# Performance work log

Measured on AMD Instinct MI355X. Metric: run time of the kernel, lower is better.

## Reference

```python
import jax, jax.numpy as jnp
import numpy as np

N_SUB, N_GLOB, S, H = 32768, 65536, 1024, 256
E_SUB, E_GLOB = 262144, 1048576


def gcn_conv(x, edge_index, W, b):
    """PyG GCNConv: add self-loops, symmetric deg^-1/2 normalization, scatter-add to targets."""
    N = x.shape[0]
    loops = jnp.arange(N, dtype=edge_index.dtype)
    row = jnp.concatenate([edge_index[0], loops])  # source
    col = jnp.concatenate([edge_index[1], loops])  # target
    deg = jax.ops.segment_sum(jnp.ones(row.shape[0], x.dtype), col, num_segments=N)
    dis = jnp.where(deg > 0, jax.lax.rsqrt(deg), 0.0)
    norm = dis[row] * dis[col]  # [E+N]
    h = x @ W  # [N,H]
    msg = h[row] * norm[:, None]  # gather + scale
    out = jax.ops.segment_sum(msg, col, num_segments=N)  # scatter-add
    return out + b


def mean_pool(x, batch, num_segments):
    sums = jax.ops.segment_sum(x, batch, num_segments=num_segments)
    cnt = jax.ops.segment_sum(jnp.ones(x.shape[0], x.dtype), batch, num_segments=num_segments)
    return sums / jnp.maximum(cnt, 1.0)[:, None]


def setup_inputs() -> dict:
    key = jax.random.key(0)
    ks = jax.random.split(key, 10)
    x_sub = jax.random.normal(ks[0], (N_SUB, H), jnp.float32)
    edge_index_sub = jax.random.randint(ks[1], (2, E_SUB), 0, N_SUB, jnp.int32)
    batch_sub = jnp.repeat(jnp.arange(S, dtype=jnp.int32), N_SUB // S)  # 32 nodes/subgraph
    sub_index = jax.random.permutation(ks[2], N_GLOB)[:S].astype(jnp.int32)  # unique targets
    x_glob = jax.random.normal(ks[3], (N_GLOB, H), jnp.float32)
    edge_index_glob = jax.random.randint(ks[4], (2, E_GLOB), 0, N_GLOB, jnp.int32)
    batch_glob = jnp.zeros((N_GLOB,), jnp.int32)
    s = 1.0 / np.sqrt(H)
    W_sub = jax.random.uniform(ks[5], (H, H), jnp.float32, -s, s)
    b_sub = jnp.zeros((H,), jnp.float32)
    W_glob = jax.random.uniform(ks[6], (H, H), jnp.float32, -s, s)
    b_glob = jnp.zeros((H,), jnp.float32)
    fc_W = jax.random.uniform(ks[7], (H, H), jnp.float32, -s, s)
    fc_b = jax.random.uniform(ks[8], (H,), jnp.float32, -s, s)
    return dict(x_sub=x_sub, edge_index_sub=edge_index_sub, batch_sub=batch_sub,
                sub_index=sub_index, x_glob=x_glob, edge_index_glob=edge_index_glob,
                batch_glob=batch_glob, W_sub=W_sub, b_sub=b_sub, W_glob=W_glob,
                b_glob=b_glob, fc_W=fc_W, fc_b=fc_b)


def reference(x_sub, edge_index_sub, batch_sub, sub_index, x_glob, edge_index_glob,
              batch_glob, W_sub, b_sub, W_glob, b_glob, fc_W, fc_b):
    # subgraph conv + per-subgraph mean pool
    h_sub = jax.nn.relu(gcn_conv(x_sub, edge_index_sub, W_sub, b_sub))
    pooled = mean_pool(h_sub, batch_sub, S)  # [S,H]
    # inject pooled subgraph embeddings into global node features
    gx = x_glob.at[sub_index].add(pooled)
    # global conv + global mean pool (batch_glob is all zeros -> 1 graph)
    gh = jax.nn.relu(gcn_conv(gx, edge_index_glob, W_glob, b_glob))
    gemb = mean_pool(gh, batch_glob, 1)  # [1,H]
    return gemb @ fc_W.T + fc_b


if __name__ == "__main__":
    out = reference(**setup_inputs())
    print(out.shape)
```

## Files before the change

### kernel.cpp

```cpp
#include <hip/hip_runtime.h>
#include <math.h>

#define NSUB  32768
#define NGLOB 65536
#define SSUB  1024
#define HD    256
#define ESUB  262144
#define EGLOB 1048576

typedef short short8 __attribute__((ext_vector_type(8)));
typedef float f32x4 __attribute__((ext_vector_type(4)));

static __device__ __forceinline__ unsigned short f2b(float f) {
  unsigned int u = __float_as_uint(f);
  unsigned int r = (u + 0x7fffu + ((u >> 16) & 1u)) >> 16;
  return (unsigned short)r;
}
static __device__ __forceinline__ float b2f(unsigned short s) {
  return __uint_as_float(((unsigned int)s) << 16);
}


__global__ void k_init(int* __restrict__ ecnt_sub, int* __restrict__ ecnt_glob,
                       int* __restrict__ inv) {
  int i = blockIdx.x * blockDim.x + threadIdx.x;
  if (i < NSUB) ecnt_sub[i] = 0;
  ecnt_glob[i] = 0;
  inv[i] = -1;
}

__global__ void k_hist2(const int* __restrict__ col_s, const int* __restrict__ col_g,
                        int* __restrict__ cnt_s, int* __restrict__ cnt_g) {
  int i = blockIdx.x * blockDim.x + threadIdx.x;
  if (i < ESUB) atomicAdd(&cnt_s[col_s[i]], 1);
  else atomicAdd(&cnt_g[col_g[i - ESUB]], 1);
}

__global__ __launch_bounds__(256) void k_scanA(const int* __restrict__ cnt_s,
                                               const int* __restrict__ cnt_g,
                                               int* __restrict__ bsum) {
  const int b = blockIdx.x;
  const int t = threadIdx.x;
  const int* cnt = (b < 32) ? cnt_s : cnt_g;
  const int chunk = (b < 32) ? b : (b - 32);
  int4 v = *(const int4*)(cnt + chunk * 1024 + t * 4);
  int s = v.x + v.y + v.z + v.w;
  __shared__ int ls[4];
#pragma unroll
  for (int d = 32; d; d >>= 1) s += __shfl_down(s, d);
  if ((t & 63) == 0) ls[t >> 6] = s;
  __syncthreads();
  if (t == 0) bsum[b] = ls[0] + ls[1] + ls[2] + ls[3];
}

__global__ void k_scanB(const int* __restrict__ bsum, int* __restrict__ bbase) {
  __shared__ int s[96];
  int t = threadIdx.x;
  if (t < 96) s[t] = bsum[t];
  __syncthreads();
  if (t == 0) { int run = 0; for (int i = 0; i < 32; ++i) { int c = s[i]; s[i] = run; run += c; } }
  if (t == 1) { int run = 0; for (int i = 32; i < 96; ++i) { int c = s[i]; s[i] = run; run += c; } }
  __syncthreads();
  if (t < 96) bbase[t] = s[t];
}

__global__ __launch_bounds__(256) void k_scanC(const int* __restrict__ cnt_s,
                                               const int* __restrict__ cnt_g,
                                               const int* __restrict__ bbase,
                                               int* __restrict__ off_s, int* __restrict__ cur_s,
                                               float* __restrict__ dis_s,
                                               int* __restrict__ off_g, int* __restrict__ cur_g,
                                               float* __restrict__ dis_g) {
  const int b = blockIdx.x;
  const int t = threadIdx.x;
  const bool isS = (b < 32);
  const int chunk = isS ? b : (b - 32);
  const int* cnt = isS ? cnt_s : cnt_g;
  int* off = isS ? off_s : off_g;
  int* cur = isS ? cur_s : cur_g;
  float* dis = isS ? dis_s : dis_g;
  const int N = isS ? NSUB : NGLOB;
  const int base = bbase[b];
  const int i0 = chunk * 1024 + t * 4;
  int4 v = *(const int4*)(cnt + i0);
  int mysum = v.x + v.y + v.z + v.w;
  __shared__ int ss[256];
  ss[t] = mysum;
  __syncthreads();
  for (int d = 1; d < 256; d <<= 1) {
    int u = (t >= d) ? ss[t - d] : 0;
    __syncthreads();
    ss[t] += u;
    __syncthreads();
  }
  int pre = base + ((t == 0) ? 0 : ss[t - 1]);
  int4 o;
  o.x = pre;
  o.y = o.x + v.x;
  o.z = o.y + v.y;
  o.w = o.z + v.z;
  *(int4*)(off + i0) = o;
  *(int4*)(cur + i0) = o;
  float4 dd = make_float4(rsqrtf((float)(v.x + 1)), rsqrtf((float)(v.y + 1)),
                          rsqrtf((float)(v.z + 1)), rsqrtf((float)(v.w + 1)));
  *(float4*)(dis + i0) = dd;
  if (i0 + 4 == N) off[N] = o.w + v.w;
}

__global__ void k_scatter2(const int* __restrict__ row_s, const int* __restrict__ col_s,
                           const int* __restrict__ row_g, const int* __restrict__ col_g,
                           int* __restrict__ cur_s, int* __restrict__ cur_g,
                           int* __restrict__ src_s, int* __restrict__ src_g) {
  int i = blockIdx.x * blockDim.x + threadIdx.x;
  if (i < ESUB) {
    int c = col_s[i];
    int slot = atomicAdd(&cur_s[c], 1);
    src_s[slot] = row_s[i];
  } else {
    int j = i - ESUB;
    int c = col_g[j];
    int slot = atomicAdd(&cur_g[c], 1);
    src_g[slot] = row_g[j];
  }
}

__global__ void k_inv(const int* __restrict__ sub_index, int* __restrict__ inv) {
  int s = blockIdx.x * blockDim.x + threadIdx.x;
  if (s < SSUB) inv[sub_index[s]] = s;
}

__global__ void k_wt(const float* __restrict__ Ws, const float* __restrict__ Wg,
                     unsigned short* __restrict__ WtS, unsigned short* __restrict__ WtG) {
  int b = blockIdx.x;
  int k = threadIdx.x;
  if (b < 256) WtS[b * 256 + k] = f2b(Ws[k * 256 + b]);
  else {
    int n = b - 256;
    WtG[n * 256 + k] = f2b(Wg[k * 256 + n]);
  }
}

template <bool ADD_POOLED>
__global__ __launch_bounds__(512) void k_gemm(const float* __restrict__ X,
                                              const unsigned short* __restrict__ Wt,
                                              unsigned short* __restrict__ Hout,
                                              const float* __restrict__ dis,
                                              const int* __restrict__ inv,
                                              const float* __restrict__ pooled) {
  __shared__ __align__(16) char As[128 * 256 * 2];
  const int t = threadIdx.x;
  const int row0 = blockIdx.x * 128;

#pragma unroll
  for (int u = 0; u < 8; ++u) {
    int idx8 = u * 512 + t;
    int r = idx8 >> 5;
    int k8 = (idx8 & 31) * 8;
    const float* p = X + (size_t)(row0 + r) * HD + k8;
    float4 a = *(const float4*)p;
    float4 b = *(const float4*)(p + 4);
    if (ADD_POOLED) {
      int piv = inv[row0 + r];
      if (piv >= 0) {
        const float* pp = pooled + (size_t)piv * HD + k8;
        float4 pa = *(const float4*)pp;
        float4 pb = *(const float4*)(pp + 4);
        a.x += pa.x; a.y += pa.y; a.z += pa.z; a.w += pa.w;
        b.x += pb.x; b.y += pb.y; b.z += pb.z; b.w += pb.w;
      }
    }
    short8 h;
    h[0] = (short)f2b(a.x); h[1] = (short)f2b(a.y);
    h[2] = (short)f2b(a.z); h[3] = (short)f2b(a.w);
    h[4] = (short)f2b(b.x); h[5] = (short)f2b(b.y);
    h[6] = (short)f2b(b.z); h[7] = (short)f2b(b.w);
    int byte = r * 512 + ((k8 * 2) ^ ((r & 7) << 4));
    *(short8*)(As + byte) = h;
  }
  __syncthreads();

  const int wid = t >> 6;
  const int lane = t & 63;
  const int wr = wid >> 2;
  const int wc = wid & 3;
  const int l15 = lane & 15;
  const int l4 = lane >> 4;

  f32x4 acc[4][4];
#pragma unroll
  for (int m = 0; m < 4; ++m)
#pragma unroll
    for (int n = 0; n < 4; ++n) acc[m][n] = (f32x4){0.f, 0.f, 0.f, 0.f};

  const unsigned short* WtB = Wt + (size_t)(wc * 64 + l15) * HD + l4 * 8;

#pragma unroll
  for (int kk = 0; kk < 8; ++kk) {
    short8 bfrag[4];
#pragma unroll
    for (int n = 0; n < 4; ++n)
      bfrag[n] = *(const short8*)(WtB + (size_t)n * 16 * HD + kk * 32);
    short8 afrag[4];
#pragma unroll
    for (int m = 0; m < 4; ++m) {
      int r = wr * 64 + m * 16 + l15;
      int ke2 = (kk * 32 + l4 * 8) * 2;
      afrag[m] = *(const short8*)(As + r * 512 + (ke2 ^ ((r & 7) << 4)));
    }
#pragma unroll
    for (int m = 0; m < 4; ++m)
#pragma unroll
      for (int n = 0; n < 4; ++n)
        acc[m][n] = __builtin_amdgcn_mfma_f32_16x16x32_bf16(afrag[m], bfrag[n], acc[m][n], 0, 0, 0);
  }

#pragma unroll
  for (int m = 0; m < 4; ++m) {
    int rbase = row0 + wr * 64 + m * 16 + l4 * 4;
    float d0 = dis[rbase + 0], d1 = dis[rbase + 1];
    float d2 = dis[rbase + 2], d3 = dis[rbase + 3];
#pragma unroll
    for (int n = 0; n < 4; ++n) {
      int c = wc * 64 + n * 16 + l15;
      unsigned short* dst = Hout + (size_t)rbase * HD + c;
      dst[0 * HD] = f2b(acc[m][n][0] * d0);
      dst[1 * HD] = f2b(acc[m][n][1] * d1);
      dst[2 * HD] = f2b(acc[m][n][2] * d2);
      dst[3 * HD] = f2b(acc[m][n][3] * d3);
    }
  }
}

__global__ __launch_bounds__(256) void k_aggpool_sub(const unsigned short* __restrict__ hh,
                                                     const int* __restrict__ off,
                                                     const int* __restrict__ src,
                                                     const float* __restrict__ dis,
                                                     const float* __restrict__ bias,
                                                     float* __restrict__ psub) {
  const int ch = threadIdx.x;
  const int bid = blockIdx.x;
  const int base = (bid >> 2) * 32 + (bid & 3) * 8;
  const float bv = bias[ch];
  float psum = 0.f;
  for (int n = 0; n < 8; ++n) {
    const int c = base + n;
    float acc = b2f(hh[(size_t)c * HD + ch]);
    int e = off[c];
    const int e1 = off[c + 1];
    for (; e + 3 < e1; e += 4) {
      int r0 = src[e], r1 = src[e + 1], r2 = src[e + 2], r3 = src[e + 3];
      acc += b2f(hh[(size_t)r0 * HD + ch]) + b2f(hh[(size_t)r1 * HD + ch]) +
             b2f(hh[(size_t)r2 * HD + ch]) + b2f(hh[(size_t)r3 * HD + ch]);
    }
    for (; e < e1; ++e) acc += b2f(hh[(size_t)src[e] * HD + ch]);
    psum += fmaxf(dis[c] * acc + bv, 0.f);
  }
  psub[(size_t)bid * HD + ch] = psum;
}

__global__ void k_redpool(const float* __restrict__ psub, float* __restrict__ pooled) {
  const int ch = threadIdx.x;
  const int s = blockIdx.x;
  float v = psub[(size_t)(4 * s + 0) * HD + ch] + psub[(size_t)(4 * s + 1) * HD + ch] +
            psub[(size_t)(4 * s + 2) * HD + ch] + psub[(size_t)(4 * s + 3) * HD + ch];
  pooled[(size_t)s * HD + ch] = v * (1.f / 32.f);
}

__global__ __launch_bounds__(256) void k_aggsum_glob(const unsigned short* __restrict__ hh,
                                                     const int* __restrict__ off,
                                                     const int* __restrict__ src,
                                                     const float* __restrict__ dis,
                                                     const float* __restrict__ bias,
                                                     float* __restrict__ pg) {
  const int ch = threadIdx.x;
  const int bid = blockIdx.x;
  const float bv = bias[ch];
  float psum = 0.f;
  for (int n = 0; n < 16; ++n) {
    const int c = bid * 16 + n;
    float acc = b2f(hh[(size_t)c * HD + ch]);
    int e = off[c];
    const int e1 = off[c + 1];
    for (; e + 3 < e1; e += 4) {
      int r0 = src[e], r1 = src[e + 1], r2 = src[e + 2], r3 = src[e + 3];
      acc += b2f(hh[(size_t)r0 * HD + ch]) + b2f(hh[(size_t)r1 * HD + ch]) +
             b2f(hh[(size_t)r2 * HD + ch]) + b2f(hh[(size_t)r3 * HD + ch]);
    }
    for (; e < e1; ++e) acc += b2f(hh[(size_t)src[e] * HD + ch]);
    psum += fmaxf(dis[c] * acc + bv, 0.f);
  }
  pg[(size_t)bid * HD + ch] = psum;
}

__global__ void k_red1(const float* __restrict__ pg, float* __restrict__ p2) {
  const int ch = threadIdx.x;
  const int b = blockIdx.x;
  float v = 0.f;
  for (int i = 0; i < 16; ++i) v += pg[(size_t)(b * 16 + i) * HD + ch];
  p2[(size_t)b * HD + ch] = v;
}

__global__ void k_final(const float* __restrict__ p2, const float* __restrict__ fcW,
                        const float* __restrict__ fcb, float* __restrict__ out) {
  __shared__ float gemb[HD];
  const int ch = threadIdx.x;
  float s = 0.f;
  for (int i = 0; i < 256; ++i) s += p2[(size_t)i * HD + ch];
  gemb[ch] = s * (1.f / 65536.f);
  __syncthreads();
  float o = fcb[ch];
  const float* wr = fcW + (size_t)ch * HD;
  for (int j = 0; j < HD; ++j) o += wr[j] * gemb[j];
  out[ch] = o;
}

extern "C" void kernel_launch(void* const* d_in, const int* in_sizes, int n_in,
                              void* d_out, int out_size, void* d_ws, size_t ws_size,
                              hipStream_t stream) {
  (void)in_sizes; (void)n_in; (void)out_size; (void)ws_size;

  const float* x_sub    = (const float*)d_in[0];
  const int*   ei_sub   = (const int*)d_in[1];
  const int*   sub_index= (const int*)d_in[3];
  const float* x_glob   = (const float*)d_in[4];
  const int*   ei_glob  = (const int*)d_in[5];
  const float* W_sub    = (const float*)d_in[7];
  const float* b_sub    = (const float*)d_in[8];
  const float* W_glob   = (const float*)d_in[9];
  const float* b_glob   = (const float*)d_in[10];
  const float* fc_W     = (const float*)d_in[11];
  const float* fc_b     = (const float*)d_in[12];
  float* out = (float*)d_out;

  char* w = (char*)d_ws;
  auto nxt = [&](size_t b) -> void* {
    void* p = (void*)w;
    w += (b + 255) & ~(size_t)255;
    return p;
  };
  unsigned short* hs   = (unsigned short*)nxt(sizeof(short) * (size_t)NSUB * HD);
  unsigned short* hg   = (unsigned short*)nxt(sizeof(short) * (size_t)NGLOB * HD);
  unsigned short* wtS  = (unsigned short*)nxt(sizeof(short) * HD * HD);
  unsigned short* wtG  = (unsigned short*)nxt(sizeof(short) * HD * HD);
  float* psub   = (float*)nxt(sizeof(float) * 4096 * HD);
  float* pooled = (float*)nxt(sizeof(float) * SSUB * HD);
  float* pg     = (float*)nxt(sizeof(float) * 4096 * HD);
  float* p2     = (float*)nxt(sizeof(float) * 256 * HD);
  int* ecnt_s   = (int*)nxt(sizeof(int) * NSUB);
  float* dis_s  = (float*)nxt(sizeof(float) * NSUB);
  int* off_s    = (int*)nxt(sizeof(int) * (NSUB + 1));
  int* cur_s    = (int*)nxt(sizeof(int) * NSUB);
  int* src_s    = (int*)nxt(sizeof(int) * ESUB);
  int* ecnt_g   = (int*)nxt(sizeof(int) * NGLOB);
  float* dis_g  = (float*)nxt(sizeof(float) * NGLOB);
  int* off_g    = (int*)nxt(sizeof(int) * (NGLOB + 1));
  int* cur_g    = (int*)nxt(sizeof(int) * NGLOB);
  int* src_g    = (int*)nxt(sizeof(int) * EGLOB);
  int* inv      = (int*)nxt(sizeof(int) * NGLOB);
  int* bsum     = (int*)nxt(sizeof(int) * 96);
  int* bbase    = (int*)nxt(sizeof(int) * 96);

  const int* row_s = ei_sub;
  const int* col_s = ei_sub + ESUB;
  const int* row_g = ei_glob;
  const int* col_g = ei_glob + EGLOB;

  k_init<<<NGLOB / 256, 256, 0, stream>>>(ecnt_s, ecnt_g, inv);
  k_hist2<<<(ESUB + EGLOB) / 256, 256, 0, stream>>>(col_s, col_g, ecnt_s, ecnt_g);
  k_scanA<<<96, 256, 0, stream>>>(ecnt_s, ecnt_g, bsum);
  k_scanB<<<1, 128, 0, stream>>>(bsum, bbase);
  k_scanC<<<96, 256, 0, stream>>>(ecnt_s, ecnt_g, bbase,
                                  off_s, cur_s, dis_s, off_g, cur_g, dis_g);
  k_scatter2<<<(ESUB + EGLOB) / 256, 256, 0, stream>>>(row_s, col_s, row_g, col_g,
                                                       cur_s, cur_g, src_s, src_g);
  k_inv<<<SSUB / 256, 256, 0, stream>>>(sub_index, inv);
  k_wt<<<512, 256, 0, stream>>>(W_sub, W_glob, wtS, wtG);

  k_gemm<false><<<NSUB / 128, 512, 0, stream>>>(x_sub, wtS, hs, dis_s, nullptr, nullptr);
  k_aggpool_sub<<<4096, 256, 0, stream>>>(hs, off_s, src_s, dis_s, b_sub, psub);
  k_redpool<<<SSUB, 256, 0, stream>>>(psub, pooled);

  k_gemm<true><<<NGLOB / 128, 512, 0, stream>>>(x_glob, wtG, hg, dis_g, inv, pooled);
  k_aggsum_glob<<<4096, 256, 0, stream>>>(hg, off_g, src_g, dis_g, b_glob, pg);
  k_red1<<<256, 256, 0, stream>>>(pg, p2);
  k_final<<<1, 256, 0, stream>>>(p2, fc_W, fc_b, out);
}
```

Baseline: 501.8 us.

## Build CSR with two-level bucket scatter and local sort; widen gather unroll

Replaces the per-node global-atomic CSR scatter with a two-pass scheme. Edges are first scattered into 64-node buckets with a packed (local col, row) word, then each bucket is sorted into final slots using shared-memory atomics. This aims to reduce global atomic contention and random writes, at the cost of an extra pass and buffer. It also vectorises the histogram loads, unrolls the aggregation gathers by 8, and adds unroll pragmas to the reductions. The packing stores the row in 16 bits, but global rows go up to 65535, which still fits.

```diff
diff --git a/kernel.cpp b/kernel.cpp
--- a/kernel.cpp
+++ b/kernel.cpp
@@ -32,8 +32,16 @@
 __global__ void k_hist2(const int* __restrict__ col_s, const int* __restrict__ col_g,
                         int* __restrict__ cnt_s, int* __restrict__ cnt_g) {
   int i = blockIdx.x * blockDim.x + threadIdx.x;
-  if (i < ESUB) atomicAdd(&cnt_s[col_s[i]], 1);
-  else atomicAdd(&cnt_g[col_g[i - ESUB]], 1);
+  if (i < ESUB / 4) {
+    int4 c = *(const int4*)(col_s + i * 4);
+    atomicAdd(&cnt_s[c.x], 1); atomicAdd(&cnt_s[c.y], 1);
+    atomicAdd(&cnt_s[c.z], 1); atomicAdd(&cnt_s[c.w], 1);
+  } else {
+    int j = i - ESUB / 4;
+    int4 c = *(const int4*)(col_g + j * 4);
+    atomicAdd(&cnt_g[c.x], 1); atomicAdd(&cnt_g[c.y], 1);
+    atomicAdd(&cnt_g[c.z], 1); atomicAdd(&cnt_g[c.w], 1);
+  }
 }
 
 __global__ __launch_bounds__(256) void k_scanA(const int* __restrict__ cnt_s,
@@ -67,18 +75,18 @@
 __global__ __launch_bounds__(256) void k_scanC(const int* __restrict__ cnt_s,
                                                const int* __restrict__ cnt_g,
                                                const int* __restrict__ bbase,
-                                               int* __restrict__ off_s, int* __restrict__ cur_s,
-                                               float* __restrict__ dis_s,
-                                               int* __restrict__ off_g, int* __restrict__ cur_g,
-                                               float* __restrict__ dis_g) {
+                                               int* __restrict__ off_s, float* __restrict__ dis_s,
+                                               int* __restrict__ bcur_s,
+                                               int* __restrict__ off_g, float* __restrict__ dis_g,
+                                               int* __restrict__ bcur_g) {
   const int b = blockIdx.x;
   const int t = threadIdx.x;
   const bool isS = (b < 32);
   const int chunk = isS ? b : (b - 32);
   const int* cnt = isS ? cnt_s : cnt_g;
   int* off = isS ? off_s : off_g;
-  int* cur = isS ? cur_s : cur_g;
   float* dis = isS ? dis_s : dis_g;
+  int* bcur = isS ? bcur_s : bcur_g;
   const int N = isS ? NSUB : NGLOB;
   const int base = bbase[b];
   const int i0 = chunk * 1024 + t * 4;
@@ -100,27 +108,51 @@
   o.z = o.y + v.y;
   o.w = o.z + v.z;
   *(int4*)(off + i0) = o;
-  *(int4*)(cur + i0) = o;
+  if ((i0 & 63) == 0) bcur[i0 >> 6] = o.x;
   float4 dd = make_float4(rsqrtf((float)(v.x + 1)), rsqrtf((float)(v.y + 1)),
                           rsqrtf((float)(v.z + 1)), rsqrtf((float)(v.w + 1)));
   *(float4*)(dis + i0) = dd;
   if (i0 + 4 == N) off[N] = o.w + v.w;
 }
 
-__global__ void k_scatter2(const int* __restrict__ row_s, const int* __restrict__ col_s,
+__global__ void k_bscatter(const int* __restrict__ row_s, const int* __restrict__ col_s,
                            const int* __restrict__ row_g, const int* __restrict__ col_g,
-                           int* __restrict__ cur_s, int* __restrict__ cur_g,
-                           int* __restrict__ src_s, int* __restrict__ src_g) {
+                           int* __restrict__ bcur_s, int* __restrict__ bcur_g,
+                           unsigned int* __restrict__ ebuf_s, unsigned int* __restrict__ ebuf_g) {
   int i = blockIdx.x * blockDim.x + threadIdx.x;
   if (i < ESUB) {
-    int c = col_s[i];
-    int slot = atomicAdd(&cur_s[c], 1);
-    src_s[slot] = row_s[i];
+    int c = col_s[i], r = row_s[i];
+    int slot = atomicAdd(&bcur_s[c >> 6], 1);
+    ebuf_s[slot] = ((unsigned)(c & 63) << 16) | (unsigned)r;
   } else {
     int j = i - ESUB;
-    int c = col_g[j];
-    int slot = atomicAdd(&cur_g[c], 1);
-    src_g[slot] = row_g[j];
+    int c = col_g[j], r = row_g[j];
+    int slot = atomicAdd(&bcur_g[c >> 6], 1);
+    ebuf_g[slot] = ((unsigned)(c & 63) << 16) | (unsigned)r;
+  }
+}
+
+__global__ __launch_bounds__(256) void k_bsort(const unsigned int* __restrict__ ebuf_s,
+                                               const unsigned int* __restrict__ ebuf_g,
+                                               const int* __restrict__ off_s,
+                                               const int* __restrict__ off_g,
+                                               int* __restrict__ src_s, int* __restrict__ src_g) {
+  __shared__ int lcur[64];
+  const int b = blockIdx.x;
+  const bool isS = (b < 512);
+  const unsigned int* ebuf = isS ? ebuf_s : ebuf_g;
+  const int* off = isS ? off_s : off_g;
+  int* src = isS ? src_s : src_g;
+  const int node0 = (isS ? b : (b - 512)) * 64;
+  const int t = threadIdx.x;
+  if (t < 64) lcur[t] = off[node0 + t];
+  __syncthreads();
+  const int base = off[node0];
+  const int end = off[node0 + 64];
+  for (int i = base + t; i < end; i += 256) {
+    unsigned e = ebuf[i];
+    int slot = atomicAdd(&lcur[e >> 16], 1);
+    src[slot] = (int)(e & 0xFFFFu);
   }
 }
 
@@ -247,10 +279,13 @@
     float acc = b2f(hh[(size_t)c * HD + ch]);
     int e = off[c];
     const int e1 = off[c + 1];
-    for (; e + 3 < e1; e += 4) {
-      int r0 = src[e], r1 = src[e + 1], r2 = src[e + 2], r3 = src[e + 3];
-      acc += b2f(hh[(size_t)r0 * HD + ch]) + b2f(hh[(size_t)r1 * HD + ch]) +
-             b2f(hh[(size_t)r2 * HD + ch]) + b2f(hh[(size_t)r3 * HD + ch]);
+    const int n8 = e + ((e1 - e) & ~7);
+    for (; e < n8; e += 8) {
+      int r[8];
+#pragma unroll
+      for (int q = 0; q < 8; ++q) r[q] = src[e + q];
+#pragma unroll
+      for (int q = 0; q < 8; ++q) acc += b2f(hh[(size_t)r[q] * HD + ch]);
     }
     for (; e < e1; ++e) acc += b2f(hh[(size_t)src[e] * HD + ch]);
     psum += fmaxf(dis[c] * acc + bv, 0.f);
@@ -281,10 +316,13 @@
     float acc = b2f(hh[(size_t)c * HD + ch]);
     int e = off[c];
     const int e1 = off[c + 1];
-    for (; e + 3 < e1; e += 4) {
-      int r0 = src[e], r1 = src[e + 1], r2 = src[e + 2], r3 = src[e + 3];
-      acc += b2f(hh[(size_t)r0 * HD + ch]) + b2f(hh[(size_t)r1 * HD + ch]) +
-             b2f(hh[(size_t)r2 * HD + ch]) + b2f(hh[(size_t)r3 * HD + ch]);
+    const int n8 = e + ((e1 - e) & ~7);
+    for (; e < n8; e += 8) {
+      int r[8];
+#pragma unroll
+      for (int q = 0; q < 8; ++q) r[q] = src[e + q];
+#pragma unroll
+      for (int q = 0; q < 8; ++q) acc += b2f(hh[(size_t)r[q] * HD + ch]);
     }
     for (; e < e1; ++e) acc += b2f(hh[(size_t)src[e] * HD + ch]);
     psum += fmaxf(dis[c] * acc + bv, 0.f);
@@ -296,6 +334,7 @@
   const int ch = threadIdx.x;
   const int b = blockIdx.x;
   float v = 0.f;
+#pragma unroll 4
   for (int i = 0; i < 16; ++i) v += pg[(size_t)(b * 16 + i) * HD + ch];
   p2[(size_t)b * HD + ch] = v;
 }
@@ -305,11 +344,13 @@
   __shared__ float gemb[HD];
   const int ch = threadIdx.x;
   float s = 0.f;
+#pragma unroll 8
   for (int i = 0; i < 256; ++i) s += p2[(size_t)i * HD + ch];
   gemb[ch] = s * (1.f / 65536.f);
   __syncthreads();
   float o = fcb[ch];
   const float* wr = fcW + (size_t)ch * HD;
+#pragma unroll 8
   for (int j = 0; j < HD; ++j) o += wr[j] * gemb[j];
   out[ch] = o;
 }
@@ -349,16 +390,18 @@
   int* ecnt_s   = (int*)nxt(sizeof(int) * NSUB);
   float* dis_s  = (float*)nxt(sizeof(float) * NSUB);
   int* off_s    = (int*)nxt(sizeof(int) * (NSUB + 1));
-  int* cur_s    = (int*)nxt(sizeof(int) * NSUB);
   int* src_s    = (int*)nxt(sizeof(int) * ESUB);
   int* ecnt_g   = (int*)nxt(sizeof(int) * NGLOB);
   float* dis_g  = (float*)nxt(sizeof(float) * NGLOB);
   int* off_g    = (int*)nxt(sizeof(int) * (NGLOB + 1));
-  int* cur_g    = (int*)nxt(sizeof(int) * NGLOB);
   int* src_g    = (int*)nxt(sizeof(int) * EGLOB);
   int* inv      = (int*)nxt(sizeof(int) * NGLOB);
   int* bsum     = (int*)nxt(sizeof(int) * 96);
   int* bbase    = (int*)nxt(sizeof(int) * 96);
+  unsigned int* ebuf_s = (unsigned int*)nxt(sizeof(int) * ESUB);
+  unsigned int* ebuf_g = (unsigned int*)nxt(sizeof(int) * EGLOB);
+  int* bcur_s   = (int*)nxt(sizeof(int) * 512);
+  int* bcur_g   = (int*)nxt(sizeof(int) * 1024);
 
   const int* row_s = ei_sub;
   const int* col_s = ei_sub + ESUB;
@@ -366,13 +409,14 @@
   const int* col_g = ei_glob + EGLOB;
 
   k_init<<<NGLOB / 256, 256, 0, stream>>>(ecnt_s, ecnt_g, inv);
-  k_hist2<<<(ESUB + EGLOB) / 256, 256, 0, stream>>>(col_s, col_g, ecnt_s, ecnt_g);
+  k_hist2<<<(ESUB + EGLOB) / 4 / 256, 256, 0, stream>>>(col_s, col_g, ecnt_s, ecnt_g);
   k_scanA<<<96, 256, 0, stream>>>(ecnt_s, ecnt_g, bsum);
   k_scanB<<<1, 128, 0, stream>>>(bsum, bbase);
   k_scanC<<<96, 256, 0, stream>>>(ecnt_s, ecnt_g, bbase,
-                                  off_s, cur_s, dis_s, off_g, cur_g, dis_g);
-  k_scatter2<<<(ESUB + EGLOB) / 256, 256, 0, stream>>>(row_s, col_s, row_g, col_g,
-                                                       cur_s, cur_g, src_s, src_g);
+                                  off_s, dis_s, bcur_s, off_g, dis_g, bcur_g);
+  k_bscatter<<<(ESUB + EGLOB) / 256, 256, 0, stream>>>(row_s, col_s, row_g, col_g,
+                                                       bcur_s, bcur_g, ebuf_s, ebuf_g);
+  k_bsort<<<512 + 1024, 256, 0, stream>>>(ebuf_s, ebuf_g, off_s, off_g, src_s, src_g);
   k_inv<<<SSUB / 256, 256, 0, stream>>>(sub_index, inv);
   k_wt<<<512, 256, 0, stream>>>(W_sub, W_glob, wtS, wtG);
 
```

Measured after the change: 685.5 us. 1.37x slower.
